# Optimization experiments

Hardware: AMD Instinct MI355X
Metric: run time of the kernel (lower is better)

The kernel has to match this reference:

```python
import jax, jax.numpy as jnp
import numpy as np

B, D, C = 8192, 128, 1000
EPS = 1e-6      # torch nn.PairwiseDistance default eps (added to the difference)
LAMBD = 0.1


def setup_inputs() -> dict:
    key = jax.random.key(0)
    k1, k2, k3 = jax.random.split(key, 3)
    return {
        "data": jax.random.normal(k1, (B, C), jnp.float32),
        "x": jax.random.normal(k2, (B, D), jnp.float32),
        "y": jax.random.randint(k3, (B,), 0, C),
    }


def _pdist_matrix(x):
    # torch PairwiseDistance(p=2): ||x_i - x_j + eps||_2, computed without
    # materializing the [B,B,D] difference tensor.
    sq = jnp.sum(x * x, axis=1)          # [B]
    s = jnp.sum(x, axis=1)               # [B]
    n = x.shape[1]
    g = x @ x.T                          # [B,B] Gram
    d2 = (sq[:, None] + sq[None, :] - 2.0 * g
          + 2.0 * EPS * (s[:, None] - s[None, :]) + n * EPS * EPS)
    return jnp.sqrt(jnp.maximum(d2, 0.0))


def reference(data, x, y):
    # cross-entropy (mean reduction, as nn.CrossEntropyLoss default)
    logp = jax.nn.log_softmax(data, axis=-1)
    loss_acc = -jnp.mean(jnp.take_along_axis(logp, y[:, None], axis=1))

    dist = _pdist_matrix(x)                       # [B,B]
    same = y[:, None] == y[None, :]               # label mask
    first_pos = jnp.argmax(same, axis=1)          # first index with same label (pos[0] in torch)
    d_pos = jnp.take_along_axis(dist, first_pos[:, None], axis=1)[:, 0]  # [B]
    d_tot = jnp.sum(dist, axis=1)                 # [B]
    loss_feature = jnp.sum(d_pos / (d_tot - d_pos))

    loss = loss_acc + LAMBD * loss_feature
    return (loss, loss_acc, loss_feature)
```

## Files before the change

kernel.cpp:

```cpp
#include <hip/hip_runtime.h>
#include <math.h>

#define B 8192
#define D 128
#define C 1000
#define EPS 1e-6f
#define LAMBD 0.1f

typedef __attribute__((ext_vector_type(8))) short short8;
typedef __attribute__((ext_vector_type(4))) float floatx4;


__device__ inline short f2bf(float f) {
    union { float f; unsigned u; } v; v.f = f;
    unsigned u = v.u;
    unsigned r = (u + 0x7fffu + ((u >> 16) & 1u)) >> 16;
    return (short)r;
}

__global__ void k_init(float* ws) {
    int t = blockIdx.x * 256 + threadIdx.x;
    if (t < 2) ws[t] = 0.f;
    if (t < B) ws[64 + 3 * B + t] = 0.f;
    int* fo = (int*)(ws + 64 + 4 * B);
    if (t < C) fo[t] = 0x7fffffff;
}

__global__ void k_rowstats(const float* __restrict__ x, const int* __restrict__ y,
                           float* ws) {
    int row = blockIdx.x * 4 + (threadIdx.x >> 6);
    int lane = threadIdx.x & 63;
    float v0 = x[row * D + lane];
    float v1 = x[row * D + 64 + lane];
    float sq = v0 * v0 + v1 * v1;
    float s = v0 + v1;
    for (int o = 32; o; o >>= 1) {
        sq += __shfl_xor(sq, o);
        s += __shfl_xor(s, o);
    }
    if (lane == 0) {
        ws[64 + row] = sq + 2.f * EPS * s;
        ws[64 + B + row] = sq - 2.f * EPS * s;
        atomicMin((int*)(ws + 64 + 4 * B) + y[row], row);
    }
}

__global__ void __launch_bounds__(256)
k_ce(const float* __restrict__ data, const int* __restrict__ y, float* ws) {
    int row = blockIdx.x * 4 + (threadIdx.x >> 6);
    int lane = threadIdx.x & 63;
    const float* dr = data + (size_t)row * C;
    const float4* dr4 = (const float4*)dr;

    float4 v[4];
    float m = -1e30f;
#pragma unroll
    for (int k = 0; k < 4; k++) {
        int idx = k * 64 + lane;
        if (idx < C / 4) {
            v[k] = dr4[idx];
            m = fmaxf(fmaxf(fmaxf(m, v[k].x), fmaxf(v[k].y, v[k].z)), v[k].w);
        }
    }
    for (int o = 32; o; o >>= 1) m = fmaxf(m, __shfl_xor(m, o));

    float sum = 0.f;
#pragma unroll
    for (int k = 0; k < 4; k++) {
        int idx = k * 64 + lane;
        if (idx < C / 4) {
            sum += __expf(v[k].x - m) + __expf(v[k].y - m) +
                   __expf(v[k].z - m) + __expf(v[k].w - m);
        }
    }
    for (int o = 32; o; o >>= 1) sum += __shfl_xor(sum, o);

    __shared__ float sp[4];
    if (lane == 0) {
        float lse = m + __logf(sum);
        sp[threadIdx.x >> 6] = lse - dr[y[row]];
    }
    __syncthreads();
    if (threadIdx.x == 0)
        atomicAdd(ws + 0, sp[0] + sp[1] + sp[2] + sp[3]);
}

__global__ void k_dpos(const float* __restrict__ x, const int* __restrict__ y,
                       float* ws) {
    int row = blockIdx.x * 4 + (threadIdx.x >> 6);
    int lane = threadIdx.x & 63;
    const int* fo = (const int*)(ws + 64 + 4 * B);
    int fp = fo[y[row]];
    float d0 = x[row * D + lane] - x[fp * D + lane] + EPS;
    float d1 = x[row * D + 64 + lane] - x[fp * D + 64 + lane] + EPS;
    float sq = d0 * d0 + d1 * d1;
    for (int o = 32; o; o >>= 1) sq += __shfl_xor(sq, o);
    if (lane == 0) ws[64 + 2 * B + row] = sqrtf(sq);
}

__global__ void __launch_bounds__(256)
k_gram_dtot(const float* __restrict__ x, float* ws) {
    int bj = blockIdx.x, bi = blockIdx.y;
    if (bj < bi) return;
    bool offdiag = (bj != bi);

    __shared__ short lA[128 * 128];
    __shared__ short lB[128 * 128];
    __shared__ float sdrow[128];
    __shared__ float sdcol[128];
    const float4* x4 = (const float4*)x;
    int t = threadIdx.x;
    int i0 = bi * 128, j0 = bj * 128;

#pragma unroll
    for (int it = 0; it < 8; ++it) {
        int idx = it * 256 + t;
        int row = idx >> 4, ch = idx & 15;
        int sw = (ch ^ (row & 7)) * 8;
        float4 a0 = x4[(size_t)(i0 + row) * 32 + ch * 2];
        float4 a1 = x4[(size_t)(i0 + row) * 32 + ch * 2 + 1];
        float4 b0 = x4[(size_t)(j0 + row) * 32 + ch * 2];
        float4 b1 = x4[(size_t)(j0 + row) * 32 + ch * 2 + 1];
        short8 sa = { f2bf(a0.x), f2bf(a0.y), f2bf(a0.z), f2bf(a0.w),
                      f2bf(a1.x), f2bf(a1.y), f2bf(a1.z), f2bf(a1.w) };
        short8 sb = { f2bf(b0.x), f2bf(b0.y), f2bf(b0.z), f2bf(b0.w),
                      f2bf(b1.x), f2bf(b1.y), f2bf(b1.z), f2bf(b1.w) };
        *(short8*)&lA[row * 128 + sw] = sa;
        *(short8*)&lB[row * 128 + sw] = sb;
    }
    if (t < 128) { sdrow[t] = 0.f; sdcol[t] = 0.f; }
    __syncthreads();

    int lane = t & 63, wid = t >> 6;
    int wm = wid >> 1, wn = wid & 1;
    int lo = lane & 15, hi = lane >> 4;

    floatx4 acc[4][4];
#pragma unroll
    for (int mr = 0; mr < 4; ++mr)
#pragma unroll
        for (int nr = 0; nr < 4; ++nr) acc[mr][nr] = (floatx4){0.f, 0.f, 0.f, 0.f};

#pragma unroll
    for (int kt = 0; kt < 4; ++kt) {
        short8 af[4], bg[4];
        int ch = kt * 4 + hi;
#pragma unroll
        for (int mr = 0; mr < 4; ++mr) {
            int r = wm * 64 + mr * 16 + lo;
            af[mr] = *(const short8*)&lA[r * 128 + (ch ^ (r & 7)) * 8];
        }
#pragma unroll
        for (int nr = 0; nr < 4; ++nr) {
            int r = wn * 64 + nr * 16 + lo;
            bg[nr] = *(const short8*)&lB[r * 128 + (ch ^ (r & 7)) * 8];
        }
#pragma unroll
        for (int mr = 0; mr < 4; ++mr)
#pragma unroll
            for (int nr = 0; nr < 4; ++nr)
                acc[mr][nr] = __builtin_amdgcn_mfma_f32_16x16x32_bf16(
                    af[mr], bg[nr], acc[mr][nr], 0, 0, 0);
    }

    const float* e = ws + 64;
    const float* f = ws + 64 + B;
    float* dtot = ws + 64 + 3 * B;
    const float deps2 = (float)D * EPS * EPS;

    float er[4][4];
#pragma unroll
    for (int mr = 0; mr < 4; ++mr)
#pragma unroll
        for (int rg = 0; rg < 4; ++rg)
            er[mr][rg] = e[i0 + wm * 64 + mr * 16 + hi * 4 + rg];
    float fc[4];
#pragma unroll
    for (int nr = 0; nr < 4; ++nr) fc[nr] = f[j0 + wn * 64 + nr * 16 + lo];

    float rs[4][4];
    float cs[4];
#pragma unroll
    for (int mr = 0; mr < 4; ++mr)
#pragma unroll
        for (int rg = 0; rg < 4; ++rg) rs[mr][rg] = 0.f;
#pragma unroll
    for (int nr = 0; nr < 4; ++nr) cs[nr] = 0.f;

#pragma unroll
    for (int mr = 0; mr < 4; ++mr)
#pragma unroll
        for (int nr = 0; nr < 4; ++nr)
#pragma unroll
            for (int rg = 0; rg < 4; ++rg) {
                float d2 = er[mr][rg] + fc[nr] - 2.f * acc[mr][nr][rg] + deps2;
                float d = sqrtf(fmaxf(d2, 0.f));
                rs[mr][rg] += d;
                cs[nr] += d;
            }

#pragma unroll
    for (int mr = 0; mr < 4; ++mr)
#pragma unroll
        for (int rg = 0; rg < 4; ++rg) {
            float v = rs[mr][rg];
            v += __shfl_xor(v, 1);
            v += __shfl_xor(v, 2);
            v += __shfl_xor(v, 4);
            v += __shfl_xor(v, 8);
            if (lo == 0) atomicAdd(&sdrow[wm * 64 + mr * 16 + hi * 4 + rg], v);
        }
    if (offdiag) {
#pragma unroll
        for (int nr = 0; nr < 4; ++nr) {
            float v = cs[nr];
            v += __shfl_xor(v, 16);
            v += __shfl_xor(v, 32);
            if (hi == 0) atomicAdd(&sdcol[wn * 64 + nr * 16 + lo], v);
        }
    }
    __syncthreads();
    if (t < 128) {
        atomicAdd(&dtot[i0 + t], sdrow[t]);
        if (offdiag) atomicAdd(&dtot[j0 + t], sdcol[t]);
    }
}

__global__ void k_feat(float* ws) {
    int i = blockIdx.x * 256 + threadIdx.x;
    float ratio = 0.f;
    if (i < B) {
        float dp = ws[64 + 2 * B + i];
        float dt = ws[64 + 3 * B + i];
        ratio = dp / (dt - dp);
    }
    for (int o = 32; o; o >>= 1) ratio += __shfl_xor(ratio, o);
    __shared__ float sm[4];
    int w = threadIdx.x >> 6;
    if ((threadIdx.x & 63) == 0) sm[w] = ratio;
    __syncthreads();
    if (threadIdx.x == 0) atomicAdd(ws + 1, sm[0] + sm[1] + sm[2] + sm[3]);
}

__global__ void k_out(const float* __restrict__ ws, float* __restrict__ out) {
    float la = ws[0] / (float)B;
    float lf = ws[1];
    out[0] = la + LAMBD * lf;
    out[1] = la;
    out[2] = lf;
}

extern "C" void kernel_launch(void* const* d_in, const int* in_sizes, int n_in,
                              void* d_out, int out_size, void* d_ws, size_t ws_size,
                              hipStream_t stream) {
    const float* data = (const float*)d_in[0];
    const float* x = (const float*)d_in[1];
    const int* y = (const int*)d_in[2];
    float* out = (float*)d_out;
    float* ws = (float*)d_ws;

    k_init<<<(B + 255) / 256, 256, 0, stream>>>(ws);
    k_rowstats<<<B / 4, 256, 0, stream>>>(x, y, ws);
    k_ce<<<B / 4, 256, 0, stream>>>(data, y, ws);
    k_dpos<<<B / 4, 256, 0, stream>>>(x, y, ws);
    k_gram_dtot<<<dim3(64, 64), 256, 0, stream>>>(x, ws);
    k_feat<<<(B + 255) / 256, 256, 0, stream>>>(ws);
    k_out<<<1, 1, 0, stream>>>(ws, out);
}
```

Before: 176.6 us.

## Precompute swizzled bf16 copy of x in rowstats and fuse final reduction kernels

The rowstats kernel now converts x to bf16 once and writes a pre-swizzled copy into the workspace. The Gram kernel then copies that copy straight into shared memory, instead of every tile reloading fp32 x and converting it again. The init kernel is replaced by two hipMemsetAsync calls, and the feat and out kernels are merged into one single-block kernel. Together these cut redundant global traffic, conversion ALU work and launch count, in exchange for an extra workspace buffer and memset API calls.

```diff
diff --git a/kernel.cpp b/kernel.cpp
--- a/kernel.cpp
+++ b/kernel.cpp
@@ -7,41 +7,41 @@
 #define EPS 1e-6f
 #define LAMBD 0.1f
 
+#define OFF_DTOT 2
+#define OFF_E (2 + B)
+#define OFF_F (2 + 2 * B)
+#define OFF_DPOS (2 + 3 * B)
+#define OFF_FO (2 + 4 * B)
+#define OFF_XBF 33792
+
 typedef __attribute__((ext_vector_type(8))) short short8;
 typedef __attribute__((ext_vector_type(4))) float floatx4;
 
-
-__device__ inline short f2bf(float f) {
+__device__ inline unsigned short f2bf(float f) {
     union { float f; unsigned u; } v; v.f = f;
     unsigned u = v.u;
-    unsigned r = (u + 0x7fffu + ((u >> 16) & 1u)) >> 16;
-    return (short)r;
-}
-
-__global__ void k_init(float* ws) {
-    int t = blockIdx.x * 256 + threadIdx.x;
-    if (t < 2) ws[t] = 0.f;
-    if (t < B) ws[64 + 3 * B + t] = 0.f;
-    int* fo = (int*)(ws + 64 + 4 * B);
-    if (t < C) fo[t] = 0x7fffffff;
-}
-
-__global__ void k_rowstats(const float* __restrict__ x, const int* __restrict__ y,
-                           float* ws) {
+    return (unsigned short)((u + 0x7fffu + ((u >> 16) & 1u)) >> 16);
+}
+
+__global__ void __launch_bounds__(256)
+k_rowstats(const float* __restrict__ x, const int* __restrict__ y, float* ws) {
     int row = blockIdx.x * 4 + (threadIdx.x >> 6);
     int lane = threadIdx.x & 63;
-    float v0 = x[row * D + lane];
-    float v1 = x[row * D + 64 + lane];
-    float sq = v0 * v0 + v1 * v1;
-    float s = v0 + v1;
+    const float2* x2 = (const float2*)x;
+    float2 v = x2[row * 64 + lane];
+    float sq = v.x * v.x + v.y * v.y;
+    float s = v.x + v.y;
     for (int o = 32; o; o >>= 1) {
         sq += __shfl_xor(sq, o);
         s += __shfl_xor(s, o);
     }
+    ushort2 p = { f2bf(v.x), f2bf(v.y) };
+    ushort2* xrow = (ushort2*)((unsigned short*)(ws + OFF_XBF) + row * 128);
+    xrow[(((lane >> 2) ^ (row & 7)) << 2) + (lane & 3)] = p;
     if (lane == 0) {
-        ws[64 + row] = sq + 2.f * EPS * s;
-        ws[64 + B + row] = sq - 2.f * EPS * s;
-        atomicMin((int*)(ws + 64 + 4 * B) + y[row], row);
+        ws[OFF_E + row] = sq + 2.f * EPS * s;
+        ws[OFF_F + row] = sq - 2.f * EPS * s;
+        atomicMin((unsigned*)(ws + OFF_FO) + y[row], (unsigned)row);
     }
 }
 
@@ -89,44 +89,34 @@
                        float* ws) {
     int row = blockIdx.x * 4 + (threadIdx.x >> 6);
     int lane = threadIdx.x & 63;
-    const int* fo = (const int*)(ws + 64 + 4 * B);
-    int fp = fo[y[row]];
+    const unsigned* fo = (const unsigned*)(ws + OFF_FO);
+    int fp = (int)fo[y[row]];
     float d0 = x[row * D + lane] - x[fp * D + lane] + EPS;
     float d1 = x[row * D + 64 + lane] - x[fp * D + 64 + lane] + EPS;
     float sq = d0 * d0 + d1 * d1;
     for (int o = 32; o; o >>= 1) sq += __shfl_xor(sq, o);
-    if (lane == 0) ws[64 + 2 * B + row] = sqrtf(sq);
+    if (lane == 0) ws[OFF_DPOS + row] = sqrtf(sq);
 }
 
 __global__ void __launch_bounds__(256)
-k_gram_dtot(const float* __restrict__ x, float* ws) {
+k_gram_dtot(float* ws) {
     int bj = blockIdx.x, bi = blockIdx.y;
     if (bj < bi) return;
     bool offdiag = (bj != bi);
 
-    __shared__ short lA[128 * 128];
-    __shared__ short lB[128 * 128];
+    __shared__ alignas(16) short lA[128 * 128];
+    __shared__ alignas(16) short lB[128 * 128];
     __shared__ float sdrow[128];
     __shared__ float sdcol[128];
-    const float4* x4 = (const float4*)x;
     int t = threadIdx.x;
     int i0 = bi * 128, j0 = bj * 128;
 
+    const short8* xb8 = (const short8*)(ws + OFF_XBF);
 #pragma unroll
     for (int it = 0; it < 8; ++it) {
         int idx = it * 256 + t;
-        int row = idx >> 4, ch = idx & 15;
-        int sw = (ch ^ (row & 7)) * 8;
-        float4 a0 = x4[(size_t)(i0 + row) * 32 + ch * 2];
-        float4 a1 = x4[(size_t)(i0 + row) * 32 + ch * 2 + 1];
-        float4 b0 = x4[(size_t)(j0 + row) * 32 + ch * 2];
-        float4 b1 = x4[(size_t)(j0 + row) * 32 + ch * 2 + 1];
-        short8 sa = { f2bf(a0.x), f2bf(a0.y), f2bf(a0.z), f2bf(a0.w),
-                      f2bf(a1.x), f2bf(a1.y), f2bf(a1.z), f2bf(a1.w) };
-        short8 sb = { f2bf(b0.x), f2bf(b0.y), f2bf(b0.z), f2bf(b0.w),
-                      f2bf(b1.x), f2bf(b1.y), f2bf(b1.z), f2bf(b1.w) };
-        *(short8*)&lA[row * 128 + sw] = sa;
-        *(short8*)&lB[row * 128 + sw] = sb;
+        ((short8*)lA)[idx] = xb8[i0 * 16 + idx];
+        ((short8*)lB)[idx] = xb8[j0 * 16 + idx];
     }
     if (t < 128) { sdrow[t] = 0.f; sdcol[t] = 0.f; }
     __syncthreads();
@@ -148,12 +138,12 @@
 #pragma unroll
         for (int mr = 0; mr < 4; ++mr) {
             int r = wm * 64 + mr * 16 + lo;
-            af[mr] = *(const short8*)&lA[r * 128 + (ch ^ (r & 7)) * 8];
+            af[mr] = *(const short8*)&lA[r * 128 + ((ch ^ (r & 7)) << 3)];
         }
 #pragma unroll
         for (int nr = 0; nr < 4; ++nr) {
             int r = wn * 64 + nr * 16 + lo;
-            bg[nr] = *(const short8*)&lB[r * 128 + (ch ^ (r & 7)) * 8];
+            bg[nr] = *(const short8*)&lB[r * 128 + ((ch ^ (r & 7)) << 3)];
         }
 #pragma unroll
         for (int mr = 0; mr < 4; ++mr)
@@ -163,9 +153,9 @@
                     af[mr], bg[nr], acc[mr][nr], 0, 0, 0);
     }
 
-    const float* e = ws + 64;
-    const float* f = ws + 64 + B;
-    float* dtot = ws + 64 + 3 * B;
+    const float* e = ws + OFF_E;
+    const float* f = ws + OFF_F;
+    float* dtot = ws + OFF_DTOT;
     const float deps2 = (float)D * EPS * EPS;
 
     float er[4][4];
@@ -173,13 +163,12 @@
     for (int mr = 0; mr < 4; ++mr)
 #pragma unroll
         for (int rg = 0; rg < 4; ++rg)
-            er[mr][rg] = e[i0 + wm * 64 + mr * 16 + hi * 4 + rg];
+            er[mr][rg] = e[i0 + wm * 64 + mr * 16 + hi * 4 + rg] + deps2;
     float fc[4];
 #pragma unroll
     for (int nr = 0; nr < 4; ++nr) fc[nr] = f[j0 + wn * 64 + nr * 16 + lo];
 
-    float rs[4][4];
-    float cs[4];
+    float rs[4][4], cs[4];
 #pragma unroll
     for (int mr = 0; mr < 4; ++mr)
 #pragma unroll
@@ -193,7 +182,7 @@
         for (int nr = 0; nr < 4; ++nr)
 #pragma unroll
             for (int rg = 0; rg < 4; ++rg) {
-                float d2 = er[mr][rg] + fc[nr] - 2.f * acc[mr][nr][rg] + deps2;
+                float d2 = er[mr][rg] + fc[nr] - 2.f * acc[mr][nr][rg];
                 float d = sqrtf(fmaxf(d2, 0.f));
                 rs[mr][rg] += d;
                 cs[nr] += d;
@@ -226,28 +215,31 @@
     }
 }
 
-__global__ void k_feat(float* ws) {
-    int i = blockIdx.x * 256 + threadIdx.x;
-    float ratio = 0.f;
-    if (i < B) {
-        float dp = ws[64 + 2 * B + i];
-        float dt = ws[64 + 3 * B + i];
-        ratio = dp / (dt - dp);
-    }
-    for (int o = 32; o; o >>= 1) ratio += __shfl_xor(ratio, o);
-    __shared__ float sm[4];
-    int w = threadIdx.x >> 6;
-    if ((threadIdx.x & 63) == 0) sm[w] = ratio;
-    __syncthreads();
-    if (threadIdx.x == 0) atomicAdd(ws + 1, sm[0] + sm[1] + sm[2] + sm[3]);
-}
-
-__global__ void k_out(const float* __restrict__ ws, float* __restrict__ out) {
-    float la = ws[0] / (float)B;
-    float lf = ws[1];
-    out[0] = la + LAMBD * lf;
-    out[1] = la;
-    out[2] = lf;
+__global__ void __launch_bounds__(1024)
+k_featout(const float* __restrict__ ws, float* __restrict__ out) {
+    int t = threadIdx.x;
+    const float* dtot = ws + OFF_DTOT;
+    const float* dpos = ws + OFF_DPOS;
+    float r = 0.f;
+#pragma unroll
+    for (int k = 0; k < B / 1024; k++) {
+        int i = k * 1024 + t;
+        float dp = dpos[i], dt = dtot[i];
+        r += dp / (dt - dp);
+    }
+    for (int o = 32; o; o >>= 1) r += __shfl_xor(r, o);
+    __shared__ float sm[16];
+    if ((t & 63) == 0) sm[t >> 6] = r;
+    __syncthreads();
+    if (t == 0) {
+        float lf = 0.f;
+#pragma unroll
+        for (int w = 0; w < 16; w++) lf += sm[w];
+        float la = ws[0] / (float)B;
+        out[0] = la + LAMBD * lf;
+        out[1] = la;
+        out[2] = lf;
+    }
 }
 
 extern "C" void kernel_launch(void* const* d_in, const int* in_sizes, int n_in,
@@ -259,11 +251,11 @@
     float* out = (float*)d_out;
     float* ws = (float*)d_ws;
 
-    k_init<<<(B + 255) / 256, 256, 0, stream>>>(ws);
+    (void)hipMemsetAsync(ws, 0, (2 + B) * sizeof(float), stream);
+    (void)hipMemsetAsync(ws + OFF_FO, 0xFF, C * sizeof(unsigned), stream);
     k_rowstats<<<B / 4, 256, 0, stream>>>(x, y, ws);
     k_ce<<<B / 4, 256, 0, stream>>>(data, y, ws);
     k_dpos<<<B / 4, 256, 0, stream>>>(x, y, ws);
-    k_gram_dtot<<<dim3(64, 64), 256, 0, stream>>>(x, ws);
-    k_feat<<<(B + 255) / 256, 256, 0, stream>>>(ws);
-    k_out<<<1, 1, 0, stream>>>(ws, out);
-}
+    k_gram_dtot<<<dim3(64, 64), 256, 0, stream>>>(ws);
+    k_featout<<<1, 1024, 0, stream>>>(ws, out);
+}
```

Result: no change. 179.6 us (+1.7%).
